# Kernel optimization log

Measured on AMD Instinct MI355X. Metric: run time of the kernel, lower is better.

The kernel has to match this reference:

```python
import jax, jax.numpy as jnp
import numpy as np

N = 50000            # num_node
E = 800000           # num edges (avg degree 16)
DIN = [128, 128, 64, 64, 32]   # nfeat, 4h, 2h, 2h, h
DOUT = [128, 64, 64, 32, 16]   # 4h, 2h, 2h, h, nclass
KAPPA = 0.9
N_FP_ITERS = 15      # fixed-point solver iterations (fixed count, jit-friendly)
N_POWER_ITERS = 50   # power iteration for spectral radius


def setup_inputs() -> dict:
    key = jax.random.key(0)
    ks = jax.random.split(key, 4 + 4 * 5)
    inp = {}
    inp["features"] = jax.random.normal(ks[0], (DIN[0], N), dtype=jnp.float32)
    inp["row"] = jax.random.randint(ks[1], (E,), 0, N, dtype=jnp.int32)
    inp["col"] = jax.random.randint(ks[2], (E,), 0, N, dtype=jnp.int32)
    inp["val"] = jax.random.uniform(ks[3], (E,), dtype=jnp.float32) * 0.1
    for i in range(5):
        din, dout = DIN[i], DOUT[i]
        inp[f"W{i}"] = jax.random.normal(ks[4 + 4 * i], (dout, dout), dtype=jnp.float32) * 0.05
        inp[f"Om{i}"] = jax.random.normal(ks[5 + 4 * i], (dout, din), dtype=jnp.float32) * (1.0 / np.sqrt(din))
        inp[f"Pw{i}"] = jax.random.normal(ks[6 + 4 * i], (dout, din), dtype=jnp.float32) * (1.0 / np.sqrt(din))
        inp[f"Pb{i}"] = jnp.zeros((dout,), dtype=jnp.float32)
    return inp


def spmm_AT(row, col, val, X):
    # A^T @ X for node-major X: [N, m]; A[row[e], col[e]] = val[e]
    return jax.ops.segment_sum(X[row] * val[:, None], col, num_segments=N)


def spmv_A(row, col, val, v):
    # (A v)[i] = sum_j A[i, j] v[j]
    return jax.ops.segment_sum(val * v[col], row, num_segments=N)


def spectral_rad(row, col, val):
    # power iteration (replaces scipy sparse eigs in get_spectral_rad)
    def step(v, _):
        w = spmv_A(row, col, val, v)
        return w / (jnp.linalg.norm(w) + 1e-12), None
    v0 = jnp.full((N,), 1.0 / np.sqrt(N), dtype=val.dtype)
    v, _ = jax.lax.scan(step, v0, None, length=N_POWER_ITERS)
    return jnp.linalg.norm(spmv_A(row, col, val, v)) + 1e-12


def project_inf_norm(W, k):
    # project each row of W onto the L1 ball of radius k (=> ||W||_inf <= k)
    a = jnp.abs(W)
    s = jnp.sort(a, axis=1)[:, ::-1]                 # descending
    cs = jnp.cumsum(s, axis=1)
    idx = jnp.arange(1, W.shape[1] + 1, dtype=W.dtype)
    nnz = jnp.sum(s - (cs - k) / idx > 0, axis=1)    # support size, >= 1
    cs_at = jnp.take_along_axis(cs, (nnz - 1)[:, None], axis=1)[:, 0]
    theta = jnp.maximum((cs_at - k) / nnz.astype(W.dtype), 0.0)
    Wp = jnp.sign(W) * jnp.maximum(a - theta[:, None], 0.0)
    return jnp.where((jnp.sum(a, axis=1) > k)[:, None], Wp, W)


def ignn_layer(row, col, val, rho, W, Om, Xt):
    # fixed point of Z = relu(W Z A + Om X A); node-major: Zt = relu(A^T Zt W^T + bt)
    Wp = project_inf_norm(W, KAPPA / rho)
    bt = spmm_AT(row, col, val, Xt @ Om.T)           # [N, dout]
    @jax.checkpoint
    def step(Z, _):
        return jax.nn.relu(spmm_AT(row, col, val, Z) @ Wp.T + bt), None
    Z, _ = jax.lax.scan(step, jnp.zeros_like(bt), None, length=N_FP_ITERS)
    return Z


def _forward(features, row, col, val, Ws, Oms, Pws, Pbs):
    rho = jax.lax.stop_gradient(spectral_rad(row, col, val))
    x = features.T                                   # node-major [N, din]
    for i in range(5):
        z = ignn_layer(row, col, val, rho, Ws[i], Oms[i], x)
        x = z + x @ Pws[i].T + Pbs[i]                # z_star + proj(x)
        if i < 4:
            x = jax.nn.elu(x)
    return x                                         # [N, nclass] (== x.T in the torch code)


def reference(features, row, col, val,
              W0, W1, W2, W3, W4,
              Om0, Om1, Om2, Om3, Om4,
              Pw0, Pw1, Pw2, Pw3, Pw4,
              Pb0, Pb1, Pb2, Pb3, Pb4):
    Ws = [W0, W1, W2, W3, W4]
    Oms = [Om0, Om1, Om2, Om3, Om4]
    Pws = [Pw0, Pw1, Pw2, Pw3, Pw4]
    Pbs = [Pb0, Pb1, Pb2, Pb3, Pb4]
    return _forward(features, row, col, val, Ws, Oms, Pws, Pbs)
```

## Files before the change

kernel.cpp:

```cpp
#include <hip/hip_runtime.h>
#include <hip/hip_fp16.h>
#include <math.h>

#define THREADS 256

static inline int ceil_div(int a, int b) { return (a + b - 1) / b; }

__device__ __forceinline__ float wave_sum_all(float v) {
#pragma unroll
  for (int m = 1; m < 64; m <<= 1) v += __shfl_xor(v, m);
  return v;
}
__device__ __forceinline__ float wave_max_all(float v) {
#pragma unroll
  for (int m = 1; m < 64; m <<= 1) v = fmaxf(v, __shfl_xor(v, m));
  return v;
}

template <int D>
__device__ __forceinline__ float2 gather_row2h(const int* __restrict__ crow,
                                               const float* __restrict__ cval,
                                               const __half* __restrict__ Z, int e0, int e1,
                                               int jj2) {
  float2 acc[8];
#pragma unroll
  for (int u = 0; u < 8; ++u) acc[u] = make_float2(0.f, 0.f);
  for (int e = e0; e < e1; e += 8) {
    int r[8];
    float v[8];
#pragma unroll
    for (int u = 0; u < 8; ++u) {
      int ee = e + u;
      bool ok = ee < e1;
      r[u] = ok ? crow[ee] : 0;
      v[u] = ok ? cval[ee] : 0.f;
    }
    float2 z[8];
#pragma unroll
    for (int u = 0; u < 8; ++u)
      z[u] = __half22float2(*(const __half2*)&Z[(size_t)r[u] * D + jj2]);
#pragma unroll
    for (int u = 0; u < 8; ++u) {
      acc[u].x += v[u] * z[u].x;
      acc[u].y += v[u] * z[u].y;
    }
  }
  float2 s01 = make_float2(acc[0].x + acc[1].x, acc[0].y + acc[1].y);
  float2 s23 = make_float2(acc[2].x + acc[3].x, acc[2].y + acc[3].y);
  float2 s45 = make_float2(acc[4].x + acc[5].x, acc[4].y + acc[5].y);
  float2 s67 = make_float2(acc[6].x + acc[7].x, acc[6].y + acc[7].y);
  return make_float2((s01.x + s23.x) + (s45.x + s67.x), (s01.y + s23.y) + (s45.y + s67.y));
}

template <int D>
__device__ __forceinline__ float2 gather_row2(const int* __restrict__ crow,
                                              const float* __restrict__ cval,
                                              const float* __restrict__ Z, int e0, int e1,
                                              int jj2) {
  float2 acc[8];
#pragma unroll
  for (int u = 0; u < 8; ++u) acc[u] = make_float2(0.f, 0.f);
  for (int e = e0; e < e1; e += 8) {
    int r[8];
    float v[8];
#pragma unroll
    for (int u = 0; u < 8; ++u) {
      int ee = e + u;
      bool ok = ee < e1;
      r[u] = ok ? crow[ee] : 0;
      v[u] = ok ? cval[ee] : 0.f;
    }
    float2 z[8];
#pragma unroll
    for (int u = 0; u < 8; ++u) z[u] = *(const float2*)&Z[(size_t)r[u] * D + jj2];
#pragma unroll
    for (int u = 0; u < 8; ++u) {
      acc[u].x += v[u] * z[u].x;
      acc[u].y += v[u] * z[u].y;
    }
  }
  float2 s01 = make_float2(acc[0].x + acc[1].x, acc[0].y + acc[1].y);
  float2 s23 = make_float2(acc[2].x + acc[3].x, acc[2].y + acc[3].y);
  float2 s45 = make_float2(acc[4].x + acc[5].x, acc[4].y + acc[5].y);
  float2 s67 = make_float2(acc[6].x + acc[7].x, acc[6].y + acc[7].y);
  return make_float2((s01.x + s23.x) + (s45.x + s67.x), (s01.y + s23.y) + (s45.y + s67.y));
}


__global__ __launch_bounds__(THREADS) void zero_i32(int* p, int n) {
  int i = blockIdx.x * THREADS + threadIdx.x;
  if (i < n) p[i] = 0;
}

__global__ __launch_bounds__(THREADS) void init_power(float* v, float* norm2, int n, float c) {
  int i = blockIdx.x * THREADS + threadIdx.x;
  if (i < n) v[i] = c;
  if (blockIdx.x == 0 && threadIdx.x < 64) norm2[threadIdx.x] = 0.f;
}

__global__ __launch_bounds__(THREADS) void hist_deg(const int* __restrict__ row,
                                                    const int* __restrict__ col,
                                                    int* rdeg, int* cdeg, int E) {
  int e = blockIdx.x * THREADS + threadIdx.x;
  if (e < E) {
    atomicAdd(&rdeg[row[e]], 1);
    atomicAdd(&cdeg[col[e]], 1);
  }
}

__global__ __launch_bounds__(THREADS) void scan1(const int* __restrict__ in, int* bsum, int L) {
  __shared__ int lds[THREADS];
  int idx = blockIdx.x * THREADS + threadIdx.x;
  lds[threadIdx.x] = (idx < L) ? in[idx] : 0;
  __syncthreads();
  for (int off = THREADS / 2; off > 0; off >>= 1) {
    if (threadIdx.x < off) lds[threadIdx.x] += lds[threadIdx.x + off];
    __syncthreads();
  }
  if (threadIdx.x == 0) bsum[blockIdx.x] = lds[0];
}

__global__ __launch_bounds__(THREADS) void scan2(int* bsum, int B) {
  __shared__ int lds[THREADS];
  int t = threadIdx.x;
  lds[t] = (t < B) ? bsum[t] : 0;
  __syncthreads();
  for (int off = 1; off < THREADS; off <<= 1) {
    int add = (t >= off) ? lds[t - off] : 0;
    __syncthreads();
    lds[t] += add;
    __syncthreads();
  }
  if (t < B) bsum[t] = (t == 0) ? 0 : lds[t - 1];
}

__global__ __launch_bounds__(THREADS) void scan3(int* data, const int* __restrict__ bsum, int L) {
  __shared__ int lds[THREADS];
  int t = threadIdx.x;
  int idx = blockIdx.x * THREADS + t;
  int v = (idx < L) ? data[idx] : 0;
  lds[t] = v;
  __syncthreads();
  for (int off = 1; off < THREADS; off <<= 1) {
    int add = (t >= off) ? lds[t - off] : 0;
    __syncthreads();
    lds[t] += add;
    __syncthreads();
  }
  if (idx < L) data[idx] = lds[t] - v + bsum[blockIdx.x];
}

__global__ __launch_bounds__(THREADS) void scatter_edges(
    const int* __restrict__ row, const int* __restrict__ col, const float* __restrict__ val,
    const int* __restrict__ rstart, int* rcur, int* csr_col, float* csr_val,
    const int* __restrict__ cstart, int* ccur, int* csc_row, float* csc_val, int E) {
  int e = blockIdx.x * THREADS + threadIdx.x;
  if (e < E) {
    int r = row[e], c = col[e];
    float v = val[e];
    int p = rstart[r] + atomicAdd(&rcur[r], 1);
    csr_col[p] = c;
    csr_val[p] = v;
    int q = cstart[c] + atomicAdd(&ccur[c], 1);
    csc_row[q] = r;
    csc_val[q] = v;
  }
}

__global__ __launch_bounds__(THREADS) void power_spmv_nn(
    const int* __restrict__ rs, const int* __restrict__ rcol, const float* __restrict__ rval,
    const float* __restrict__ vin, float* __restrict__ vout, int n) {
  int gid = blockIdx.x * THREADS + threadIdx.x;
  int node = gid >> 2;
  int sl = gid & 3;
  if (node >= n) return;
  int e0 = rs[node], e1 = rs[node + 1];
  float a0 = 0.f, a1 = 0.f, a2 = 0.f, a3 = 0.f;
  for (int e = e0 + sl; e < e1; e += 16) {
    int ee1 = e + 4, ee2 = e + 8, ee3 = e + 12;
    bool k1 = ee1 < e1, k2 = ee2 < e1, k3 = ee3 < e1;
    int r0 = rcol[e];
    int r1 = k1 ? rcol[ee1] : 0;
    int r2 = k2 ? rcol[ee2] : 0;
    int r3 = k3 ? rcol[ee3] : 0;
    float v0 = rval[e];
    float v1 = k1 ? rval[ee1] : 0.f;
    float v2 = k2 ? rval[ee2] : 0.f;
    float v3 = k3 ? rval[ee3] : 0.f;
    a0 += v0 * vin[r0];
    a1 += v1 * vin[r1];
    a2 += v2 * vin[r2];
    a3 += v3 * vin[r3];
  }
  float w = (a0 + a1) + (a2 + a3);
  w += __shfl_xor(w, 1);
  w += __shfl_xor(w, 2);
  if (sl == 0) vout[node] = w;
}

__global__ __launch_bounds__(THREADS) void norm2_pair(const float* __restrict__ u,
                                                      const float* __restrict__ w,
                                                      float* norm2, int n) {
  int i = blockIdx.x * THREADS + threadIdx.x;
  float a = (i < n) ? u[i] : 0.f;
  float b = (i < n) ? w[i] : 0.f;
  float sa = wave_sum_all(a * a);
  float sb = wave_sum_all(b * b);
  __shared__ float pa[4], pb[4];
  if ((threadIdx.x & 63) == 0) {
    pa[threadIdx.x >> 6] = sa;
    pb[threadIdx.x >> 6] = sb;
  }
  __syncthreads();
  if (threadIdx.x == 0) atomicAdd(&norm2[0], pa[0] + pa[1] + pa[2] + pa[3]);
  if (threadIdx.x == 64) atomicAdd(&norm2[1], pb[0] + pb[1] + pb[2] + pb[3]);
}


__global__ __launch_bounds__(256) void transpose_feat(const float* __restrict__ in,
                                                      float* __restrict__ out, int n) {
  __shared__ float tile[32][33];
  int bx = blockIdx.x;
  int by = blockIdx.y;
  int x = bx * 32 + threadIdx.x;
  for (int dy = threadIdx.y; dy < 32; dy += 8) {
    int y = by * 32 + dy;
    tile[dy][threadIdx.x] = (x < n) ? in[(size_t)y * n + x] : 0.f;
  }
  __syncthreads();
  for (int dy = threadIdx.y; dy < 32; dy += 8) {
    int node = bx * 32 + dy;
    int feat = by * 32 + threadIdx.x;
    if (node < n) out[(size_t)node * 128 + feat] = tile[threadIdx.x][dy];
  }
}

__global__ __launch_bounds__(THREADS) void transpose_small(const float* __restrict__ in,
                                                           float* __restrict__ out, int rows,
                                                           int cols) {
  int idx = blockIdx.x * THREADS + threadIdx.x;
  if (idx < rows * cols) {
    int r = idx / cols, c = idx % cols;
    out[c * rows + r] = in[idx];
  }
}

template <int D>
__global__ __launch_bounds__(64) void project_row(const float* __restrict__ W,
                                                  float* __restrict__ WpT,
                                                  const float* __restrict__ norm2) {
  int o = blockIdx.x;
  int l = threadIdx.x;
  float rho = sqrtf(norm2[0] / norm2[1]) + 1e-12f;
  float k = 0.9f / rho;
  float a0 = (l < D) ? W[o * D + l] : 0.f;
  float a1 = (64 + l < D) ? W[o * D + 64 + l] : 0.f;
  float ab0 = fabsf(a0), ab1 = fabsf(a1);
  float s = wave_sum_all(ab0 + ab1);
  float mx = wave_max_all(fmaxf(ab0, ab1));
  float w0 = a0, w1 = a1;
  if (s > k) {
    float lo = 0.f, hi = mx;
    for (int it = 0; it < 50; ++it) {
      float mid = 0.5f * (lo + hi);
      float g = wave_sum_all(fmaxf(ab0 - mid, 0.f) + fmaxf(ab1 - mid, 0.f));
      if (g > k) lo = mid; else hi = mid;
    }
    float theta = 0.5f * (lo + hi);
    w0 = copysignf(fmaxf(ab0 - theta, 0.f), a0);
    w1 = copysignf(fmaxf(ab1 - theta, 0.f), a1);
  }
  if (l < D) WpT[l * D + o] = w0;
  if (64 + l < D) WpT[(64 + l) * D + o] = w1;
}

template <int DOUT>
__global__ __launch_bounds__(THREADS, 8) void spmm_bt(
    const int* __restrict__ cstart, const int* __restrict__ crow, const float* __restrict__ cval,
    const float* __restrict__ X, float* __restrict__ bt, __half* __restrict__ Zinit, int n) {
  constexpr int HD = DOUT / 2;
  int idx = blockIdx.x * THREADS + threadIdx.x;
  int node = idx / HD;
  int jj2 = (idx % HD) * 2;
  if (node >= n) return;
  int e0 = cstart[node], e1 = cstart[node + 1];
  float2 acc = gather_row2<DOUT>(crow, cval, X, e0, e1, jj2);
  size_t o = (size_t)node * DOUT + jj2;
  *(float2*)&bt[o] = acc;
  *(__half2*)&Zinit[o] = __floats2half2_rn(fmaxf(acc.x, 0.f), fmaxf(acc.y, 0.f));
}

template <int DOUT, int NB>
__global__ __launch_bounds__(THREADS, 8) void fp_step(
    const int* __restrict__ cstart, const int* __restrict__ crow, const float* __restrict__ cval,
    const __half* __restrict__ Zin, const float* __restrict__ WpT, const float* __restrict__ bt,
    __half* __restrict__ Zout, int n) {
  constexpr int TO = DOUT / 4;
  constexpr int TN = THREADS / TO;
  constexpr int NT = NB / TN;
  static_assert(NT >= 1, "NB too small");
  __shared__ float sT[NB][DOUT + 2];
  const int node0 = blockIdx.x * NB;
  const int tid = threadIdx.x;
  {
    constexpr int HD = DOUT / 2;
    constexpr int LG = THREADS / HD;
    const int jj2 = (tid % HD) * 2;
    const int lg = tid / HD;
    for (int nn = lg; nn < NB; nn += LG) {
      int node = node0 + nn;
      float2 acc = make_float2(0.f, 0.f);
      if (node < n) {
        int e0 = cstart[node], e1 = cstart[node + 1];
        acc = gather_row2h<DOUT>(crow, cval, Zin, e0, e1, jj2);
      }
      *(float2*)&sT[nn][jj2] = acc;
    }
  }
  __syncthreads();
  const int o4 = tid % TO, tg = tid / TO;
  const int o0 = o4 * 4;
  float acc[NT][4];
#pragma unroll
  for (int a = 0; a < NT; ++a) acc[a][0] = acc[a][1] = acc[a][2] = acc[a][3] = 0.f;
  for (int jz = 0; jz < DOUT; ++jz) {
    const float4 w4 = *(const float4*)&WpT[jz * DOUT + o0];
#pragma unroll
    for (int a = 0; a < NT; ++a) {
      float sv = sT[tg * NT + a][jz];
      acc[a][0] += sv * w4.x;
      acc[a][1] += sv * w4.y;
      acc[a][2] += sv * w4.z;
      acc[a][3] += sv * w4.w;
    }
  }
#pragma unroll
  for (int a = 0; a < NT; ++a) {
    int node = node0 + tg * NT + a;
    if (node < n) {
      const float4 b4 = *(const float4*)&bt[(size_t)node * DOUT + o0];
      float zx = fmaxf(acc[a][0] + b4.x, 0.f);
      float zy = fmaxf(acc[a][1] + b4.y, 0.f);
      float zz = fmaxf(acc[a][2] + b4.z, 0.f);
      float zw = fmaxf(acc[a][3] + b4.w, 0.f);
      size_t o = (size_t)node * DOUT + o0;
      *(__half2*)&Zout[o] = __floats2half2_rn(zx, zy);
      *(__half2*)&Zout[o + 2] = __floats2half2_rn(zz, zw);
    }
  }
}

template <int DOUT, int NB>
__global__ __launch_bounds__(THREADS) void dense_gemm(
    const float* __restrict__ X, int din, const float* __restrict__ MT,
    const float* __restrict__ bias, const __half* __restrict__ Addh, int act,
    float* __restrict__ Out, int n) {
  constexpr int TO = DOUT / 4;
  constexpr int TN = THREADS / TO;
  constexpr int NT = NB / TN;
  __shared__ float xs[NB][129];
  const int node0 = blockIdx.x * NB;
  const int tid = threadIdx.x;
  for (int idx = tid; idx < NB * din; idx += THREADS) {
    int nn = idx / din, j = idx % din;
    int node = node0 + nn;
    xs[nn][j] = (node < n) ? X[(size_t)node * din + j] : 0.f;
  }
  __syncthreads();
  const int o4 = tid % TO, tg = tid / TO;
  const int o0 = o4 * 4;
  float acc[NT][4];
#pragma unroll
  for (int a = 0; a < NT; ++a) acc[a][0] = acc[a][1] = acc[a][2] = acc[a][3] = 0.f;
  for (int j = 0; j < din; ++j) {
    const float4 m4 = *(const float4*)&MT[j * DOUT + o0];
#pragma unroll
    for (int a = 0; a < NT; ++a) {
      float sv = xs[tg * NT + a][j];
      acc[a][0] += sv * m4.x;
      acc[a][1] += sv * m4.y;
      acc[a][2] += sv * m4.z;
      acc[a][3] += sv * m4.w;
    }
  }
#pragma unroll
  for (int a = 0; a < NT; ++a) {
    int node = node0 + tg * NT + a;
    if (node < n) {
      float4 r;
      r.x = acc[a][0]; r.y = acc[a][1]; r.z = acc[a][2]; r.w = acc[a][3];
      if (bias) {
        r.x += bias[o0]; r.y += bias[o0 + 1]; r.z += bias[o0 + 2]; r.w += bias[o0 + 3];
      }
      if (Addh) {
        size_t o = (size_t)node * DOUT + o0;
        float2 a01 = __half22float2(*(const __half2*)&Addh[o]);
        float2 a23 = __half22float2(*(const __half2*)&Addh[o + 2]);
        r.x += a01.x; r.y += a01.y; r.z += a23.x; r.w += a23.y;
      }
      if (act == 1) {
        r.x = (r.x > 0.f) ? r.x : expm1f(r.x);
        r.y = (r.y > 0.f) ? r.y : expm1f(r.y);
        r.z = (r.z > 0.f) ? r.z : expm1f(r.z);
        r.w = (r.w > 0.f) ? r.w : expm1f(r.w);
      }
      *(float4*)&Out[(size_t)node * DOUT + o0] = r;
    }
  }
}


static void launch_project(int dout, const float* W, float* WpT, const float* norm2,
                           hipStream_t s) {
  switch (dout) {
    case 128: project_row<128><<<128, 64, 0, s>>>(W, WpT, norm2); break;
    case 64: project_row<64><<<64, 64, 0, s>>>(W, WpT, norm2); break;
    case 32: project_row<32><<<32, 64, 0, s>>>(W, WpT, norm2); break;
    case 16: project_row<16><<<16, 64, 0, s>>>(W, WpT, norm2); break;
  }
}

static void launch_spmm_bt(int dout, const int* cs, const int* cr, const float* cv,
                           const float* X, float* bt, __half* Zi, int n, hipStream_t s) {
  int g = ceil_div(n * dout / 2, THREADS);
  switch (dout) {
    case 128: spmm_bt<128><<<g, THREADS, 0, s>>>(cs, cr, cv, X, bt, Zi, n); break;
    case 64: spmm_bt<64><<<g, THREADS, 0, s>>>(cs, cr, cv, X, bt, Zi, n); break;
    case 32: spmm_bt<32><<<g, THREADS, 0, s>>>(cs, cr, cv, X, bt, Zi, n); break;
    case 16: spmm_bt<16><<<g, THREADS, 0, s>>>(cs, cr, cv, X, bt, Zi, n); break;
  }
}

static void launch_fp_step(int dout, const int* cs, const int* cr, const float* cv,
                           const __half* Zin, const float* WpT, const float* bt, __half* Zout,
                           int n, hipStream_t s) {
  switch (dout) {
    case 128: fp_step<128, 16><<<ceil_div(n, 16), THREADS, 0, s>>>(cs, cr, cv, Zin, WpT, bt, Zout, n); break;
    case 64: fp_step<64, 16><<<ceil_div(n, 16), THREADS, 0, s>>>(cs, cr, cv, Zin, WpT, bt, Zout, n); break;
    case 32: fp_step<32, 32><<<ceil_div(n, 32), THREADS, 0, s>>>(cs, cr, cv, Zin, WpT, bt, Zout, n); break;
    case 16: fp_step<16, 64><<<ceil_div(n, 64), THREADS, 0, s>>>(cs, cr, cv, Zin, WpT, bt, Zout, n); break;
  }
}

static void launch_dense_gemm(int dout, const float* X, int din, const float* MT,
                              const float* bias, const __half* Addh, int act, float* Out, int n,
                              hipStream_t s) {
  switch (dout) {
    case 128: dense_gemm<128, 32><<<ceil_div(n, 32), THREADS, 0, s>>>(X, din, MT, bias, Addh, act, Out, n); break;
    case 64: dense_gemm<64, 32><<<ceil_div(n, 32), THREADS, 0, s>>>(X, din, MT, bias, Addh, act, Out, n); break;
    case 32: dense_gemm<32, 32><<<ceil_div(n, 32), THREADS, 0, s>>>(X, din, MT, bias, Addh, act, Out, n); break;
    case 16: dense_gemm<16, 64><<<ceil_div(n, 64), THREADS, 0, s>>>(X, din, MT, bias, Addh, act, Out, n); break;
  }
}

extern "C" void kernel_launch(void* const* d_in, const int* in_sizes, int n_in, void* d_out,
                              int out_size, void* d_ws, size_t ws_size, hipStream_t stream) {
  const float* features = (const float*)d_in[0];
  const int* row = (const int*)d_in[1];
  const int* col = (const int*)d_in[2];
  const float* val = (const float*)d_in[3];
  const int N = in_sizes[0] / 128;
  const int E = in_sizes[1];
  static const int DIN[5] = {128, 128, 64, 64, 32};
  static const int DOUT[5] = {128, 64, 64, 32, 16};

  char* base = (char*)d_ws;
  size_t off = 0;
  auto alloc = [&](size_t bytes) -> void* {
    off = (off + 255) & ~(size_t)255;
    void* p = (void*)(base + off);
    off += bytes;
    return p;
  };

  int* rstart = (int*)alloc((size_t)(N + 1) * 4);
  int* cstart = (int*)alloc((size_t)(N + 1) * 4);
  int* rcur = (int*)alloc((size_t)N * 4);
  int* ccur = (int*)alloc((size_t)N * 4);
  int* bsum = (int*)alloc(256 * 4);
  float* norm2 = (float*)alloc(64 * 4);
  float* v_a = (float*)alloc((size_t)N * 4);
  float* v_b = (float*)alloc((size_t)N * 4);
  int* csr_col = (int*)alloc((size_t)E * 4);
  float* csr_val = (float*)alloc((size_t)E * 4);
  int* csc_row = (int*)alloc((size_t)E * 4);
  float* csc_val = (float*)alloc((size_t)E * 4);
  float* WpT = (float*)alloc(16384 * 4);
  float* OmT = (float*)alloc(16384 * 4);
  float* PwT = (float*)alloc(16384 * 4);
  float* x0 = (float*)alloc((size_t)N * 128 * 4);
  float* x1 = (float*)alloc((size_t)N * 128 * 4);
  float* xom = (float*)alloc((size_t)N * 128 * 4);
  float* btb = (float*)alloc((size_t)N * 128 * 4);
  __half* z_a = (__half*)alloc((size_t)N * 128 * 2);
  __half* z_b = (__half*)alloc((size_t)N * 128 * 2);

  const int gN = ceil_div(N, THREADS);
  const int gE = ceil_div(E, THREADS);
  const int L = N + 1;
  const int B = ceil_div(L, THREADS);

  zero_i32<<<ceil_div(N + 1, THREADS), THREADS, 0, stream>>>(rstart, N + 1);
  zero_i32<<<ceil_div(N + 1, THREADS), THREADS, 0, stream>>>(cstart, N + 1);
  zero_i32<<<gN, THREADS, 0, stream>>>(rcur, N);
  zero_i32<<<gN, THREADS, 0, stream>>>(ccur, N);
  init_power<<<gN, THREADS, 0, stream>>>(v_a, norm2, N, (float)(1.0 / sqrt((double)N)));
  hist_deg<<<gE, THREADS, 0, stream>>>(row, col, rstart, cstart, E);
  scan1<<<B, THREADS, 0, stream>>>(rstart, bsum, L);
  scan2<<<1, THREADS, 0, stream>>>(bsum, B);
  scan3<<<B, THREADS, 0, stream>>>(rstart, bsum, L);
  scan1<<<B, THREADS, 0, stream>>>(cstart, bsum, L);
  scan2<<<1, THREADS, 0, stream>>>(bsum, B);
  scan3<<<B, THREADS, 0, stream>>>(cstart, bsum, L);
  scatter_edges<<<gE, THREADS, 0, stream>>>(row, col, val, rstart, rcur, csr_col, csr_val,
                                            cstart, ccur, csc_row, csc_val, E);

  {
    dim3 grid(ceil_div(N, 32), 4);
    dim3 block(32, 8);
    transpose_feat<<<grid, block, 0, stream>>>(features, x0, N);
  }

  {
    int g4 = ceil_div(N * 4, THREADS);
    for (int k = 1; k <= 51; ++k) {
      const float* vin = (k & 1) ? v_a : v_b;
      float* vout = (k & 1) ? v_b : v_a;
      power_spmv_nn<<<g4, THREADS, 0, stream>>>(rstart, csr_col, csr_val, vin, vout, N);
    }
    norm2_pair<<<gN, THREADS, 0, stream>>>(v_b, v_a, norm2, N);
  }

  float* xcur = x0;
  float* xnext = x1;
  for (int i = 0; i < 5; ++i) {
    const int din = DIN[i], dout = DOUT[i];
    const float* W = (const float*)d_in[4 + 4 * i];
    const float* Om = (const float*)d_in[5 + 4 * i];
    const float* Pw = (const float*)d_in[6 + 4 * i];
    const float* Pb = (const float*)d_in[7 + 4 * i];

    transpose_small<<<ceil_div(dout * din, THREADS), THREADS, 0, stream>>>(Om, OmT, dout, din);
    transpose_small<<<ceil_div(dout * din, THREADS), THREADS, 0, stream>>>(Pw, PwT, dout, din);
    launch_project(dout, W, WpT, norm2, stream);

    launch_dense_gemm(dout, xcur, din, OmT, nullptr, nullptr, 0, xom, N, stream);
    launch_spmm_bt(dout, cstart, csc_row, csc_val, xom, btb, z_a, N, stream);
    for (int s = 0; s < 14; ++s) {
      const __half* zin = (s & 1) ? z_b : z_a;
      __half* zout = (s & 1) ? z_a : z_b;
      launch_fp_step(dout, cstart, csc_row, csc_val, zin, WpT, btb, zout, N, stream);
    }
    float* outp = (i < 4) ? xnext : (float*)d_out;
    launch_dense_gemm(dout, xcur, din, PwT, Pb, z_a, (i < 4) ? 1 : 0, outp, N, stream);
    float* t = xcur; xcur = xnext; xnext = t;
  }
}
```

Before: 4.880 ms.

## Widen sparse gathers to 16-byte loads and store bias term in half precision

The gather helpers now load 8 half values (fp_step) or 4 floats (spmm_bt) per thread with a single 16-byte load instead of 2 elements per load. Each thread in fp_step handles exactly one node, and block node counts grow for the smaller widths. The bt bias buffer is stored as fp16, halving its reads in every fixed-point iteration. The wider loads use fewer lanes per row, which may lower parallelism for low-degree nodes, and the fp16 bias adds rounding error.

```diff
diff --git a/kernel.cpp b/kernel.cpp
--- a/kernel.cpp
+++ b/kernel.cpp
@@ -18,72 +18,72 @@
 }
 
 template <int D>
-__device__ __forceinline__ float2 gather_row2h(const int* __restrict__ crow,
-                                               const float* __restrict__ cval,
-                                               const __half* __restrict__ Z, int e0, int e1,
-                                               int jj2) {
-  float2 acc[8];
-#pragma unroll
-  for (int u = 0; u < 8; ++u) acc[u] = make_float2(0.f, 0.f);
-  for (int e = e0; e < e1; e += 8) {
-    int r[8];
-    float v[8];
-#pragma unroll
-    for (int u = 0; u < 8; ++u) {
+__device__ __forceinline__ void gather_row8h(const int* __restrict__ crow,
+                                             const float* __restrict__ cval,
+                                             const __half* __restrict__ Z, int e0, int e1,
+                                             int jj8, float* __restrict__ acc) {
+#pragma unroll
+  for (int k = 0; k < 8; ++k) acc[k] = 0.f;
+  for (int e = e0; e < e1; e += 4) {
+    int r[4];
+    float v[4];
+#pragma unroll
+    for (int u = 0; u < 4; ++u) {
       int ee = e + u;
       bool ok = ee < e1;
       r[u] = ok ? crow[ee] : 0;
       v[u] = ok ? cval[ee] : 0.f;
     }
-    float2 z[8];
-#pragma unroll
-    for (int u = 0; u < 8; ++u)
-      z[u] = __half22float2(*(const __half2*)&Z[(size_t)r[u] * D + jj2]);
-#pragma unroll
-    for (int u = 0; u < 8; ++u) {
-      acc[u].x += v[u] * z[u].x;
-      acc[u].y += v[u] * z[u].y;
-    }
-  }
-  float2 s01 = make_float2(acc[0].x + acc[1].x, acc[0].y + acc[1].y);
-  float2 s23 = make_float2(acc[2].x + acc[3].x, acc[2].y + acc[3].y);
-  float2 s45 = make_float2(acc[4].x + acc[5].x, acc[4].y + acc[5].y);
-  float2 s67 = make_float2(acc[6].x + acc[7].x, acc[6].y + acc[7].y);
-  return make_float2((s01.x + s23.x) + (s45.x + s67.x), (s01.y + s23.y) + (s45.y + s67.y));
+    float4 z[4];
+#pragma unroll
+    for (int u = 0; u < 4; ++u) z[u] = *(const float4*)&Z[(size_t)r[u] * D + jj8];
+#pragma unroll
+    for (int u = 0; u < 4; ++u) {
+      const __half2* h = (const __half2*)&z[u];
+      float2 f0 = __half22float2(h[0]);
+      float2 f1 = __half22float2(h[1]);
+      float2 f2 = __half22float2(h[2]);
+      float2 f3 = __half22float2(h[3]);
+      acc[0] += v[u] * f0.x;
+      acc[1] += v[u] * f0.y;
+      acc[2] += v[u] * f1.x;
+      acc[3] += v[u] * f1.y;
+      acc[4] += v[u] * f2.x;
+      acc[5] += v[u] * f2.y;
+      acc[6] += v[u] * f3.x;
+      acc[7] += v[u] * f3.y;
+    }
+  }
 }
 
 template <int D>
-__device__ __forceinline__ float2 gather_row2(const int* __restrict__ crow,
-                                              const float* __restrict__ cval,
-                                              const float* __restrict__ Z, int e0, int e1,
-                                              int jj2) {
-  float2 acc[8];
-#pragma unroll
-  for (int u = 0; u < 8; ++u) acc[u] = make_float2(0.f, 0.f);
-  for (int e = e0; e < e1; e += 8) {
-    int r[8];
-    float v[8];
-#pragma unroll
-    for (int u = 0; u < 8; ++u) {
+__device__ __forceinline__ void gather_row4f(const int* __restrict__ crow,
+                                             const float* __restrict__ cval,
+                                             const float* __restrict__ Z, int e0, int e1,
+                                             int jj4, float* __restrict__ acc) {
+#pragma unroll
+  for (int k = 0; k < 4; ++k) acc[k] = 0.f;
+  for (int e = e0; e < e1; e += 4) {
+    int r[4];
+    float v[4];
+#pragma unroll
+    for (int u = 0; u < 4; ++u) {
       int ee = e + u;
       bool ok = ee < e1;
       r[u] = ok ? crow[ee] : 0;
       v[u] = ok ? cval[ee] : 0.f;
     }
-    float2 z[8];
-#pragma unroll
-    for (int u = 0; u < 8; ++u) z[u] = *(const float2*)&Z[(size_t)r[u] * D + jj2];
-#pragma unroll
-    for (int u = 0; u < 8; ++u) {
-      acc[u].x += v[u] * z[u].x;
-      acc[u].y += v[u] * z[u].y;
-    }
-  }
-  float2 s01 = make_float2(acc[0].x + acc[1].x, acc[0].y + acc[1].y);
-  float2 s23 = make_float2(acc[2].x + acc[3].x, acc[2].y + acc[3].y);
-  float2 s45 = make_float2(acc[4].x + acc[5].x, acc[4].y + acc[5].y);
-  float2 s67 = make_float2(acc[6].x + acc[7].x, acc[6].y + acc[7].y);
-  return make_float2((s01.x + s23.x) + (s45.x + s67.x), (s01.y + s23.y) + (s45.y + s67.y));
+    float4 z[4];
+#pragma unroll
+    for (int u = 0; u < 4; ++u) z[u] = *(const float4*)&Z[(size_t)r[u] * D + jj4];
+#pragma unroll
+    for (int u = 0; u < 4; ++u) {
+      acc[0] += v[u] * z[u].x;
+      acc[1] += v[u] * z[u].y;
+      acc[2] += v[u] * z[u].z;
+      acc[3] += v[u] * z[u].w;
+    }
+  }
 }
 
 
@@ -277,45 +277,49 @@
 template <int DOUT>
 __global__ __launch_bounds__(THREADS, 8) void spmm_bt(
     const int* __restrict__ cstart, const int* __restrict__ crow, const float* __restrict__ cval,
-    const float* __restrict__ X, float* __restrict__ bt, __half* __restrict__ Zinit, int n) {
-  constexpr int HD = DOUT / 2;
+    const float* __restrict__ X, __half* __restrict__ bt, __half* __restrict__ Zinit, int n) {
+  constexpr int QD = DOUT / 4;
   int idx = blockIdx.x * THREADS + threadIdx.x;
-  int node = idx / HD;
-  int jj2 = (idx % HD) * 2;
+  int node = idx / QD;
+  int jj4 = (idx % QD) * 4;
   if (node >= n) return;
   int e0 = cstart[node], e1 = cstart[node + 1];
-  float2 acc = gather_row2<DOUT>(crow, cval, X, e0, e1, jj2);
-  size_t o = (size_t)node * DOUT + jj2;
-  *(float2*)&bt[o] = acc;
-  *(__half2*)&Zinit[o] = __floats2half2_rn(fmaxf(acc.x, 0.f), fmaxf(acc.y, 0.f));
+  float acc[4];
+  gather_row4f<DOUT>(crow, cval, X, e0, e1, jj4, acc);
+  size_t o = (size_t)node * DOUT + jj4;
+  *(__half2*)&bt[o] = __floats2half2_rn(acc[0], acc[1]);
+  *(__half2*)&bt[o + 2] = __floats2half2_rn(acc[2], acc[3]);
+  *(__half2*)&Zinit[o] = __floats2half2_rn(fmaxf(acc[0], 0.f), fmaxf(acc[1], 0.f));
+  *(__half2*)&Zinit[o + 2] = __floats2half2_rn(fmaxf(acc[2], 0.f), fmaxf(acc[3], 0.f));
 }
 
 template <int DOUT, int NB>
 __global__ __launch_bounds__(THREADS, 8) void fp_step(
     const int* __restrict__ cstart, const int* __restrict__ crow, const float* __restrict__ cval,
-    const __half* __restrict__ Zin, const float* __restrict__ WpT, const float* __restrict__ bt,
+    const __half* __restrict__ Zin, const float* __restrict__ WpT, const __half* __restrict__ bt,
     __half* __restrict__ Zout, int n) {
   constexpr int TO = DOUT / 4;
   constexpr int TN = THREADS / TO;
   constexpr int NT = NB / TN;
-  static_assert(NT >= 1, "NB too small");
-  __shared__ float sT[NB][DOUT + 2];
+  constexpr int TPN = DOUT / 8;
+  constexpr int LG = THREADS / TPN;
+  static_assert(NB == LG, "one node per thread");
+  __shared__ float sT[NB][DOUT + 4];
   const int node0 = blockIdx.x * NB;
   const int tid = threadIdx.x;
   {
-    constexpr int HD = DOUT / 2;
-    constexpr int LG = THREADS / HD;
-    const int jj2 = (tid % HD) * 2;
-    const int lg = tid / HD;
-    for (int nn = lg; nn < NB; nn += LG) {
-      int node = node0 + nn;
-      float2 acc = make_float2(0.f, 0.f);
-      if (node < n) {
-        int e0 = cstart[node], e1 = cstart[node + 1];
-        acc = gather_row2h<DOUT>(crow, cval, Zin, e0, e1, jj2);
-      }
-      *(float2*)&sT[nn][jj2] = acc;
-    }
+    const int jj8 = (tid % TPN) * 8;
+    const int nn = tid / TPN;
+    const int node = node0 + nn;
+    float acc[8];
+#pragma unroll
+    for (int k = 0; k < 8; ++k) acc[k] = 0.f;
+    if (node < n) {
+      int e0 = cstart[node], e1 = cstart[node + 1];
+      gather_row8h<DOUT>(crow, cval, Zin, e0, e1, jj8, acc);
+    }
+    *(float4*)&sT[nn][jj8] = make_float4(acc[0], acc[1], acc[2], acc[3]);
+    *(float4*)&sT[nn][jj8 + 4] = make_float4(acc[4], acc[5], acc[6], acc[7]);
   }
   __syncthreads();
   const int o4 = tid % TO, tg = tid / TO;
@@ -338,12 +342,13 @@
   for (int a = 0; a < NT; ++a) {
     int node = node0 + tg * NT + a;
     if (node < n) {
-      const float4 b4 = *(const float4*)&bt[(size_t)node * DOUT + o0];
-      float zx = fmaxf(acc[a][0] + b4.x, 0.f);
-      float zy = fmaxf(acc[a][1] + b4.y, 0.f);
-      float zz = fmaxf(acc[a][2] + b4.z, 0.f);
-      float zw = fmaxf(acc[a][3] + b4.w, 0.f);
       size_t o = (size_t)node * DOUT + o0;
+      float2 b01 = __half22float2(*(const __half2*)&bt[o]);
+      float2 b23 = __half22float2(*(const __half2*)&bt[o + 2]);
+      float zx = fmaxf(acc[a][0] + b01.x, 0.f);
+      float zy = fmaxf(acc[a][1] + b01.y, 0.f);
+      float zz = fmaxf(acc[a][2] + b23.x, 0.f);
+      float zw = fmaxf(acc[a][3] + b23.y, 0.f);
       *(__half2*)&Zout[o] = __floats2half2_rn(zx, zy);
       *(__half2*)&Zout[o + 2] = __floats2half2_rn(zz, zw);
     }
@@ -421,8 +426,8 @@
 }
 
 static void launch_spmm_bt(int dout, const int* cs, const int* cr, const float* cv,
-                           const float* X, float* bt, __half* Zi, int n, hipStream_t s) {
-  int g = ceil_div(n * dout / 2, THREADS);
+                           const float* X, __half* bt, __half* Zi, int n, hipStream_t s) {
+  int g = ceil_div(n * dout / 4, THREADS);
   switch (dout) {
     case 128: spmm_bt<128><<<g, THREADS, 0, s>>>(cs, cr, cv, X, bt, Zi, n); break;
     case 64: spmm_bt<64><<<g, THREADS, 0, s>>>(cs, cr, cv, X, bt, Zi, n); break;
@@ -432,13 +437,13 @@
 }
 
 static void launch_fp_step(int dout, const int* cs, const int* cr, const float* cv,
-                           const __half* Zin, const float* WpT, const float* bt, __half* Zout,
+                           const __half* Zin, const float* WpT, const __half* bt, __half* Zout,
                            int n, hipStream_t s) {
   switch (dout) {
     case 128: fp_step<128, 16><<<ceil_div(n, 16), THREADS, 0, s>>>(cs, cr, cv, Zin, WpT, bt, Zout, n); break;
-    case 64: fp_step<64, 16><<<ceil_div(n, 16), THREADS, 0, s>>>(cs, cr, cv, Zin, WpT, bt, Zout, n); break;
-    case 32: fp_step<32, 32><<<ceil_div(n, 32), THREADS, 0, s>>>(cs, cr, cv, Zin, WpT, bt, Zout, n); break;
-    case 16: fp_step<16, 64><<<ceil_div(n, 64), THREADS, 0, s>>>(cs, cr, cv, Zin, WpT, bt, Zout, n); break;
+    case 64: fp_step<64, 32><<<ceil_div(n, 32), THREADS, 0, s>>>(cs, cr, cv, Zin, WpT, bt, Zout, n); break;
+    case 32: fp_step<32, 64><<<ceil_div(n, 64), THREADS, 0, s>>>(cs, cr, cv, Zin, WpT, bt, Zout, n); break;
+    case 16: fp_step<16, 128><<<ceil_div(n, 128), THREADS, 0, s>>>(cs, cr, cv, Zin, WpT, bt, Zout, n); break;
   }
 }
 
@@ -491,7 +496,7 @@
   float* x0 = (float*)alloc((size_t)N * 128 * 4);
   float* x1 = (float*)alloc((size_t)N * 128 * 4);
   float* xom = (float*)alloc((size_t)N * 128 * 4);
-  float* btb = (float*)alloc((size_t)N * 128 * 4);
+  __half* btb = (__half*)alloc((size_t)N * 128 * 2);
   __half* z_a = (__half*)alloc((size_t)N * 128 * 2);
   __half* z_b = (__half*)alloc((size_t)N * 128 * 2);
 
```

Result: slower. 11.51 ms (+135.9%).
